# Optimization experiments

Measured on AMD Instinct MI355X. Metric: run time of the kernel, lower is better.

## Reference

```python
import jax, jax.numpy as jnp
import numpy as np

B, S1, S2, H1, H2, HID = 8, 512, 512, 128, 128, 128

def setup_inputs() -> dict:
    key = jax.random.key(0)
    ks = jax.random.split(key, 8)
    return {
        "query": jax.random.normal(ks[0], (B, S1, H1), jnp.float32),
        "key": jax.random.normal(ks[1], (B, S2, H2), jnp.float32),
        "value": jax.random.normal(ks[2], (B, S2, H2), jnp.float32),
        "q_mask": jax.random.randint(ks[3], (B, S1), 0, 2, jnp.int32),
        "k_mask": jax.random.randint(ks[4], (B, S2), 0, 2, jnp.int32),
        # init_weights: Linear weight ~ N(0, 0.01), bias = 0
        "W1": jax.random.normal(ks[5], (HID, H1 + H2), jnp.float32) * 0.01,
        "b1": jnp.zeros((HID,), jnp.float32),
        "W2": jax.random.normal(ks[6], (1, HID), jnp.float32) * 0.01,
        "b2": jnp.zeros((1,), jnp.float32),
    }

def reference(query, key, value, q_mask, k_mask, W1, b1, W2, b2):
    h1 = query.shape[-1]
    # Linear on concat([q,k]) == q @ W1[:, :h1].T + k @ W1[:, h1:].T + b1
    qp = jnp.einsum('bsd,hd->bsh', query, W1[:, :h1]) + b1   # [B,S1,HID]
    kp = jnp.einsum('btd,hd->bth', key, W1[:, h1:])          # [B,S2,HID]
    h = jax.nn.relu(qp[:, :, None, :] + kp[:, None, :, :])   # [B,S1,S2,HID]
    s = jnp.einsum('bsth,h->bst', h, W2[0]) + b2[0]          # [B,S1,S2]
    mask = (q_mask[:, :, None] * k_mask[:, None, :]) > 0     # [B,S1,S2]
    A = jnp.where(mask, jnp.exp(s), 0.0)                     # masked_fill(-inf).exp()
    A_sum = jnp.clip(jnp.sum(A, axis=-1, keepdims=True), 2e-15, None)
    attn = A / A_sum
    return jnp.einsum('bst,btd->bsd', attn, value)           # [B,S1,H2]
```

## Files before the change

### kernel.cpp

```cpp
#include <hip/hip_runtime.h>

#define S 512
#define H 128
#define NROW 4096
#define TI 4

__global__ __launch_bounds__(256) void w1t_kernel(const float* __restrict__ W1,
                                                  float* __restrict__ w1T) {
  __shared__ float t[32][33];
  const int d0 = (blockIdx.x & 7) * 32;
  const int h0 = (blockIdx.x >> 3) * 32;
  const int tx = threadIdx.x & 31, ty = threadIdx.x >> 5;
  #pragma unroll
  for (int r = 0; r < 4; r++)
    t[ty + r * 8][tx] = W1[(h0 + ty + r * 8) * 256 + d0 + tx];
  __syncthreads();
  #pragma unroll
  for (int r = 0; r < 4; r++)
    w1T[(size_t)(d0 + ty + r * 8) * H + h0 + tx] = t[tx][ty + r * 8];
}

__global__ __launch_bounds__(256, 8) void proj_kernel(
    const float* __restrict__ query, const float* __restrict__ key,
    const float* __restrict__ w1T, const float* __restrict__ b1,
    const float* __restrict__ W2, const float* __restrict__ b2,
    float* __restrict__ qp, float* __restrict__ kp2,
    float* __restrict__ qw, float* __restrict__ kw)
{
  const int bid = blockIdx.x;
  const bool isq = bid < 512;
  const float* __restrict__ src = isq ? query : key;
  const int rbase = (isq ? bid : bid - 512) * 8;
  const int doff = isq ? 0 : 128;
  const int tid = threadIdx.x;
  const int w = __builtin_amdgcn_readfirstlane(tid >> 6);
  const int lane = tid & 63;
  const int r0w = rbase + w * 2;

  float acc[2][2];
  float2 bv = make_float2(0.f, 0.f);
  if (isq) bv = *(const float2*)(b1 + 2 * lane);
  acc[0][0] = bv.x; acc[0][1] = bv.y;
  acc[1][0] = bv.x; acc[1][1] = bv.y;

  #pragma unroll 1
  for (int dc = 0; dc < 128; dc += 16) {
    float qs[2][16];
    #pragma unroll
    for (int r = 0; r < 2; r++) {
      const float* sp = src + (size_t)(r0w + r) * H + dc;
      #pragma unroll
      for (int u = 0; u < 16; u++) qs[r][u] = sp[u];
    }
    float2 wv[16];
    #pragma unroll
    for (int dd = 0; dd < 16; dd++)
      wv[dd] = *(const float2*)(w1T + (size_t)(doff + dc + dd) * H + 2 * lane);
    #pragma unroll
    for (int dd = 0; dd < 16; dd++) {
      acc[0][0] = __builtin_fmaf(qs[0][dd], wv[dd].x, acc[0][0]);
      acc[0][1] = __builtin_fmaf(qs[0][dd], wv[dd].y, acc[0][1]);
      acc[1][0] = __builtin_fmaf(qs[1][dd], wv[dd].x, acc[1][0]);
      acc[1][1] = __builtin_fmaf(qs[1][dd], wv[dd].y, acc[1][1]);
    }
  }

  const float2 w2p = *(const float2*)(W2 + 2 * lane);
  const float b2v = b2[0];
  #pragma unroll
  for (int r = 0; r < 2; r++) {
    float t = acc[r][0] * w2p.x + acc[r][1] * w2p.y;
    #pragma unroll
    for (int m = 1; m <= 32; m <<= 1) t += __shfl_xor(t, m, 64);
    if (lane == 0) {
      if (isq) qw[r0w + r] = 0.5f * t + b2v;
      else     kw[r0w + r] = 0.5f * t;
    }
  }

  if (isq) {
    #pragma unroll
    for (int r = 0; r < 2; r++)
      *(float2*)(qp + (size_t)(r0w + r) * H + 2 * lane) =
          make_float2(acc[r][0], acc[r][1]);
  } else {
    #pragma unroll
    for (int r = 0; r < 2; r++)
      *(float2*)(kp2 + ((size_t)(lane >> 3) * NROW + (r0w + r)) * 16 +
                 (lane & 7) * 2) = make_float2(acc[r][0], acc[r][1]);
  }
}

__global__ __launch_bounds__(512, 8) void attn_kernel(
    const float* __restrict__ qp, const float* __restrict__ kp2,
    const float* __restrict__ qw, const float* __restrict__ kw,
    const float* __restrict__ value, const int* __restrict__ q_mask,
    const int* __restrict__ k_mask, const float* __restrict__ W2,
    float* __restrict__ out)
{
  __shared__ float aT[8][64][4];
  __shared__ float numw[8][TI][132];
  __shared__ float denw[8][TI];

  const int it = blockIdx.x;
  const int r0 = it * TI;
  const int b  = r0 >> 9;
  const int tid = threadIdx.x;
  const int w = __builtin_amdgcn_readfirstlane(tid >> 6);
  const int lane = tid & 63;
  const int jg = (b << 9) + (w << 6) + lane;
  const int km = k_mask[jg];
  const float kwj = kw[jg];

  float s[TI];
  #pragma unroll
  for (int i = 0; i < TI; i++) s[i] = 0.f;

  #pragma unroll 1
  for (int hb = 0; hb < 8; hb++) {
    float kr[16];
    {
      const float* __restrict__ kk = kp2 + (((size_t)hb * NROW + jg) << 4);
      #pragma unroll
      for (int u = 0; u < 4; u++) *(float4*)&kr[u * 4] = ((const float4*)kk)[u];
    }
    float w2r[16];
    #pragma unroll
    for (int u = 0; u < 16; u++) w2r[u] = W2[hb * 16 + u];

    #pragma unroll 1
    for (int ip = 0; ip < TI; ip += 2) {
      float q0[16], q1[16];
      {
        const float* __restrict__ qa = qp + (size_t)(r0 + ip) * H + hb * 16;
        #pragma unroll
        for (int u = 0; u < 16; u++) { q0[u] = qa[u]; q1[u] = qa[H + u]; }
      }
      float s0 = s[ip], s1 = s[ip + 1];
      #pragma unroll
      for (int u = 0; u < 16; u++) {
        const float t0 = q0[u] + kr[u];
        const float t1 = q1[u] + kr[u];
        s0 = __builtin_fmaf(fabsf(t0), w2r[u], s0);
        s1 = __builtin_fmaf(fabsf(t1), w2r[u], s1);
      }
      s[ip] = s0; s[ip + 1] = s1;
    }
  }

  float a[TI];
  #pragma unroll
  for (int i = 0; i < TI; i++) {
    const float qws = qw[r0 + i];
    const int qm = q_mask[r0 + i];
    a[i] = (km > 0 && qm > 0) ? __expf(__builtin_fmaf(0.5f, s[i], qws + kwj))
                              : 0.f;
  }
  *(float4*)&aT[w][lane][0] = make_float4(a[0], a[1], a[2], a[3]);

  const int lj = lane >> 5, lh = lane & 31;
  float nr[TI][4];
  float dden[TI];
  #pragma unroll
  for (int i = 0; i < TI; i++) {
    nr[i][0] = 0.f; nr[i][1] = 0.f; nr[i][2] = 0.f; nr[i][3] = 0.f;
    dden[i] = 0.f;
  }
  const float* __restrict__ vbase =
      value + ((size_t)b * S + (w << 6)) * H;

  #pragma unroll 1
  for (int js = 0; js < 32; js++) {
    const int j = js * 2 + lj;
    const float4 vv = *(const float4*)(vbase + (size_t)j * H + lh * 4);
    const float4 a4 = *(const float4*)&aT[w][j][0];
    const float av[4] = {a4.x, a4.y, a4.z, a4.w};
    #pragma unroll
    for (int i = 0; i < TI; i++) {
      nr[i][0] = __builtin_fmaf(av[i], vv.x, nr[i][0]);
      nr[i][1] = __builtin_fmaf(av[i], vv.y, nr[i][1]);
      nr[i][2] = __builtin_fmaf(av[i], vv.z, nr[i][2]);
      nr[i][3] = __builtin_fmaf(av[i], vv.w, nr[i][3]);
      dden[i] += av[i];
    }
  }
  #pragma unroll
  for (int i = 0; i < TI; i++) {
    #pragma unroll
    for (int k = 0; k < 4; k++) nr[i][k] += __shfl_xor(nr[i][k], 32, 64);
    dden[i] += __shfl_xor(dden[i], 32, 64);
  }
  if (lj == 0) {
    #pragma unroll
    for (int i = 0; i < TI; i++)
      *(float4*)&numw[w][i][lh * 4] =
          make_float4(nr[i][0], nr[i][1], nr[i][2], nr[i][3]);
    if (lane == 0) {
      #pragma unroll
      for (int i = 0; i < TI; i++) denw[w][i] = dden[i];
    }
  }
  __syncthreads();

  {
    const int i = w & 3, half = w >> 2;
    float acc = 0.f, den = 0.f;
    #pragma unroll
    for (int ww = 0; ww < 8; ww++) {
      acc += numw[ww][i][half * 64 + lane];
      den += denw[ww][i];
    }
    const float inv = 1.f / fmaxf(den, 2e-15f);
    out[(size_t)(r0 + i) * H + half * 64 + lane] = acc * inv;
  }
}

extern "C" void kernel_launch(void* const* d_in, const int* in_sizes, int n_in,
                              void* d_out, int out_size, void* d_ws, size_t ws_size,
                              hipStream_t stream)
{
  (void)in_sizes; (void)n_in; (void)out_size; (void)ws_size;
  const float* query  = (const float*)d_in[0];
  const float* key    = (const float*)d_in[1];
  const float* value  = (const float*)d_in[2];
  const int*   q_mask = (const int*)d_in[3];
  const int*   k_mask = (const int*)d_in[4];
  const float* W1     = (const float*)d_in[5];
  const float* b1     = (const float*)d_in[6];
  const float* W2     = (const float*)d_in[7];
  const float* b2     = (const float*)d_in[8];
  float* out = (float*)d_out;

  float* ws   = (float*)d_ws;
  float* w1T  = ws;
  float* qp   = w1T + 256 * H;
  float* kp2  = qp + (size_t)NROW * H;
  float* qw   = kp2 + (size_t)NROW * H;
  float* kw   = qw + NROW;

  w1t_kernel<<<32, 256, 0, stream>>>(W1, w1T);
  proj_kernel<<<1024, 256, 0, stream>>>(query, key, w1T, b1, W2, b2,
                                        qp, kp2, qw, kw);
  attn_kernel<<<1024, 512, 0, stream>>>(qp, kp2, qw, kw, value, q_mask,
                                        k_mask, W2, out);
}
```

Before: 128.7 us.

## Reblock projection rows per wave and relayout key projections for coalesced loads

The projection kernel now computes 8 rows per wave instead of 2, so each W1 column load is reused across more rows, and it launches 256 blocks instead of 1024. The key-projection buffer moves to a new interleaved layout so that in the attention kernel each lane's float4 loads across the wave fall on consecutive addresses. The aim is to raise weight reuse in the projection and make the inner attention loop's key loads fully coalesced. In exchange, proj uses more registers and fewer blocks, which may leave the GPU underfilled.

New measurement: 128.2 us. No clear change (-0.4%).

```diff
diff --git a/kernel.cpp b/kernel.cpp
--- a/kernel.cpp
+++ b/kernel.cpp
@@ -4,6 +4,7 @@
 #define H 128
 #define NROW 4096
 #define TI 4
+
 
 __global__ __launch_bounds__(256) void w1t_kernel(const float* __restrict__ W1,
                                                   float* __restrict__ w1T) {
@@ -20,55 +21,56 @@
     w1T[(size_t)(d0 + ty + r * 8) * H + h0 + tx] = t[tx][ty + r * 8];
 }
 
-__global__ __launch_bounds__(256, 8) void proj_kernel(
+__global__ __launch_bounds__(256) void proj_kernel(
     const float* __restrict__ query, const float* __restrict__ key,
     const float* __restrict__ w1T, const float* __restrict__ b1,
     const float* __restrict__ W2, const float* __restrict__ b2,
-    float* __restrict__ qp, float* __restrict__ kp2,
+    float* __restrict__ qp, float* __restrict__ kp3,
     float* __restrict__ qw, float* __restrict__ kw)
 {
   const int bid = blockIdx.x;
-  const bool isq = bid < 512;
+  const bool isq = bid < 128;
   const float* __restrict__ src = isq ? query : key;
-  const int rbase = (isq ? bid : bid - 512) * 8;
+  const int rbase = (isq ? bid : bid - 128) * 32;
   const int doff = isq ? 0 : 128;
   const int tid = threadIdx.x;
   const int w = __builtin_amdgcn_readfirstlane(tid >> 6);
   const int lane = tid & 63;
-  const int r0w = rbase + w * 2;
-
-  float acc[2][2];
+  const int r0w = rbase + w * 8;
+
+  float acc[8][2];
   float2 bv = make_float2(0.f, 0.f);
   if (isq) bv = *(const float2*)(b1 + 2 * lane);
-  acc[0][0] = bv.x; acc[0][1] = bv.y;
-  acc[1][0] = bv.x; acc[1][1] = bv.y;
+  #pragma unroll
+  for (int r = 0; r < 8; r++) { acc[r][0] = bv.x; acc[r][1] = bv.y; }
 
   #pragma unroll 1
-  for (int dc = 0; dc < 128; dc += 16) {
-    float qs[2][16];
-    #pragma unroll
-    for (int r = 0; r < 2; r++) {
+  for (int dc = 0; dc < 128; dc += 8) {
+    float qs[8][8];
+    #pragma unroll
+    for (int r = 0; r < 8; r++) {
       const float* sp = src + (size_t)(r0w + r) * H + dc;
       #pragma unroll
-      for (int u = 0; u < 16; u++) qs[r][u] = sp[u];
-    }
-    float2 wv[16];
-    #pragma unroll
-    for (int dd = 0; dd < 16; dd++)
+      for (int u = 0; u < 8; u++) qs[r][u] = sp[u];
+    }
+    float2 wv[8];
+    #pragma unroll
+    for (int dd = 0; dd < 8; dd++)
       wv[dd] = *(const float2*)(w1T + (size_t)(doff + dc + dd) * H + 2 * lane);
     #pragma unroll
-    for (int dd = 0; dd < 16; dd++) {
-      acc[0][0] = __builtin_fmaf(qs[0][dd], wv[dd].x, acc[0][0]);
-      acc[0][1] = __builtin_fmaf(qs[0][dd], wv[dd].y, acc[0][1]);
-      acc[1][0] = __builtin_fmaf(qs[1][dd], wv[dd].x, acc[1][0]);
-      acc[1][1] = __builtin_fmaf(qs[1][dd], wv[dd].y, acc[1][1]);
+    for (int dd = 0; dd < 8; dd++) {
+      #pragma unroll
+      for (int r = 0; r < 8; r++) {
+        acc[r][0] = __builtin_fmaf(qs[r][dd], wv[dd].x, acc[r][0]);
+        acc[r][1] = __builtin_fmaf(qs[r][dd], wv[dd].y, acc[r][1]);
+      }
     }
   }
 
   const float2 w2p = *(const float2*)(W2 + 2 * lane);
   const float b2v = b2[0];
   #pragma unroll
-  for (int r = 0; r < 2; r++) {
+  for (int r = 0; r < 8; r++) {
     float t = acc[r][0] * w2p.x + acc[r][1] * w2p.y;
     #pragma unroll
     for (int m = 1; m <= 32; m <<= 1) t += __shfl_xor(t, m, 64);
@@ -80,19 +82,23 @@
 
   if (isq) {
     #pragma unroll
-    for (int r = 0; r < 2; r++)
+    for (int r = 0; r < 8; r++)
       *(float2*)(qp + (size_t)(r0w + r) * H + 2 * lane) =
           make_float2(acc[r][0], acc[r][1]);
   } else {
-    #pragma unroll
-    for (int r = 0; r < 2; r++)
-      *(float2*)(kp2 + ((size_t)(lane >> 3) * NROW + (r0w + r)) * 16 +
-                 (lane & 7) * 2) = make_float2(acc[r][0], acc[r][1]);
+    const int hb = lane >> 3, hq = (lane >> 1) & 3, hm = (lane & 1) * 2;
+    #pragma unroll
+    for (int r = 0; r < 8; r++) {
+      const int j = r0w + r;
+      float* dst = kp3 +
+          ((((size_t)hb * 64 + (j >> 6)) * 4 + hq) * 64 + (j & 63)) * 4 + hm;
+      *(float2*)dst = make_float2(acc[r][0], acc[r][1]);
+    }
   }
 }
 
 __global__ __launch_bounds__(512, 8) void attn_kernel(
-    const float* __restrict__ qp, const float* __restrict__ kp2,
+    const float* __restrict__ qp, const float* __restrict__ kp3,
     const float* __restrict__ qw, const float* __restrict__ kw,
     const float* __restrict__ value, const int* __restrict__ q_mask,
     const int* __restrict__ k_mask, const float* __restrict__ W2,
@@ -109,6 +115,7 @@
   const int w = __builtin_amdgcn_readfirstlane(tid >> 6);
   const int lane = tid & 63;
   const int jg = (b << 9) + (w << 6) + lane;
+  const int jb = (b << 3) + w;
   const int km = k_mask[jg];
   const float kwj = kw[jg];
 
@@ -118,12 +125,13 @@
 
   #pragma unroll 1
   for (int hb = 0; hb < 8; hb++) {
+    const float* __restrict__ kk =
+        kp3 + ((size_t)(hb * 64 + jb)) * 1024 + lane * 4;
     float kr[16];
-    {
-      const float* __restrict__ kk = kp2 + (((size_t)hb * NROW + jg) << 4);
-      #pragma unroll
-      for (int u = 0; u < 4; u++) *(float4*)&kr[u * 4] = ((const float4*)kk)[u];
-    }
+    *(float4*)&kr[0]  = *(const float4*)(kk);
+    *(float4*)&kr[4]  = *(const float4*)(kk + 256);
+    *(float4*)&kr[8]  = *(const float4*)(kk + 512);
+    *(float4*)&kr[12] = *(const float4*)(kk + 768);
     float w2r[16];
     #pragma unroll
     for (int u = 0; u < 16; u++) w2r[u] = W2[hb * 16 + u];
@@ -234,13 +242,13 @@
   float* ws   = (float*)d_ws;
   float* w1T  = ws;
   float* qp   = w1T + 256 * H;
-  float* kp2  = qp + (size_t)NROW * H;
-  float* qw   = kp2 + (size_t)NROW * H;
+  float* kp3  = qp + (size_t)NROW * H;
+  float* qw   = kp3 + (size_t)NROW * H;
   float* kw   = qw + NROW;
 
   w1t_kernel<<<32, 256, 0, stream>>>(W1, w1T);
-  proj_kernel<<<1024, 256, 0, stream>>>(query, key, w1T, b1, W2, b2,
-                                        qp, kp2, qw, kw);
-  attn_kernel<<<1024, 512, 0, stream>>>(qp, kp2, qw, kw, value, q_mask,
+  proj_kernel<<<256, 256, 0, stream>>>(query, key, w1T, b1, W2, b2,
+                                       qp, kp3, qw, kw);
+  attn_kernel<<<1024, 512, 0, stream>>>(qp, kp3, qw, kw, value, q_mask,
                                         k_mask, W2, out);
 }
```
